# Optimization experiments

Measured on AMD Instinct MI355X. Metric: run time of the kernel, lower is better.

The kernel has to match this reference:

```python
import jax, jax.numpy as jnp
import numpy as np

T, B, E, H = 2048, 4, 1024, 16
HD = E // H
SCALE = HD ** -0.5


def setup_inputs() -> dict:
    key = jax.random.key(0)
    k1, k2, k3 = jax.random.split(key, 3)
    # xavier-ish scaling on weights for numerical sanity
    inputs = jax.random.normal(k1, (T, B, E), dtype=jnp.float32)
    in_proj_weight = jax.random.normal(k2, (3 * E, E), dtype=jnp.float32) * (2.0 / (4 * E)) ** 0.5
    out_proj_weight = jax.random.normal(k3, (E, E), dtype=jnp.float32) * (1.0 / E) ** 0.5
    return {"inputs": inputs, "in_proj_weight": in_proj_weight, "out_proj_weight": out_proj_weight}


def reference(inputs, in_proj_weight, out_proj_weight):
    t, b, e = inputs.shape
    # fused QKV projection: [T,B,E] @ [E,3E] -> [T, B*H, 3, HD]
    qkv = jnp.einsum('tbe,fe->tbf', inputs, in_proj_weight)
    qkv = qkv.reshape(t, b * H, 3, HD)
    q, k, v = qkv[:, :, 0, :], qkv[:, :, 1, :], qkv[:, :, 2, :]  # [T, B*H, HD]
    # scaled attention scores per (batch*head): [B*H, T, T]
    scores = SCALE * jnp.einsum('tnd,snd->nts', q, k)
    probs = jax.nn.softmax(scores, axis=-1)
    # dropout p=0.0 -> identity
    ctx = jnp.einsum('nts,snd->tnd', probs, v).reshape(t, b, e)
    # output projection (applied to attention context, matching intended math / backward)
    return jnp.einsum('tbe,oe->tbo', ctx, out_proj_weight)
```

## Files before the change

### kernel.cpp

```cpp
#include <hip/hip_runtime.h>
#include <stdint.h>
#include <stddef.h>


typedef __attribute__((ext_vector_type(8))) short bf16x8;
typedef __attribute__((ext_vector_type(4))) float f32x4;
typedef __attribute__((ext_vector_type(4))) unsigned int u32x4;

#define MFMA16(a, b, c) __builtin_amdgcn_mfma_f32_16x16x32_bf16((a), (b), (c), 0, 0, 0)

__device__ __forceinline__ unsigned short f2bf(float f) {
  unsigned u = __builtin_bit_cast(unsigned, f);
  u += 0x7fffu + ((u >> 16) & 1u);
  return (unsigned short)(u >> 16);
}

__device__ __forceinline__ float fast_exp2(float x) {
#if __has_builtin(__builtin_amdgcn_exp2f)
  return __builtin_amdgcn_exp2f(x);
#else
  return exp2f(x);
#endif
}

__device__ __forceinline__ unsigned cvtpk(float lo, float hi) {
  unsigned r;
  asm volatile("v_cvt_pk_bf16_f32 %0, %1, %2" : "=v"(r) : "v"(lo), "v"(hi));
  return r;
}

__device__ __forceinline__ void lane_swap32(unsigned &a, unsigned &b) {
#if __has_builtin(__builtin_amdgcn_permlane32_swap)
  auto r = __builtin_amdgcn_permlane32_swap(a, b, false, false);
  a = r[0]; b = r[1];
#else
  const bool hi = (threadIdx.x & 32) != 0;
  unsigned sa = (unsigned)__shfl_xor((int)a, 32, 64);
  unsigned sb = (unsigned)__shfl_xor((int)b, 32, 64);
  unsigned na = hi ? sb : a;
  unsigned nb = hi ? b : sa;
  a = na; b = nb;
#endif
}

__device__ __forceinline__ void lane_swap16(unsigned &a, unsigned &b) {
#if __has_builtin(__builtin_amdgcn_permlane16_swap)
  auto r = __builtin_amdgcn_permlane16_swap(a, b, false, false);
  a = r[0]; b = r[1];
#else
  const bool odd = (threadIdx.x & 16) != 0;
  unsigned sa = (unsigned)__shfl_xor((int)a, 16, 64);
  unsigned sb = (unsigned)__shfl_xor((int)b, 16, 64);
  unsigned na = odd ? sb : a;
  unsigned nb = odd ? b : sa;
  a = na; b = nb;
#endif
}

__device__ __forceinline__ void gload_lds16(const void* g, void* l) {
  __builtin_amdgcn_global_load_lds((const __attribute__((address_space(1))) void*)g,
                                   (__attribute__((address_space(3))) void*)l,
                                   16, 0, 0);
}

__global__ __launch_bounds__(256) void k_cvt(const float* __restrict__ src,
                                             unsigned short* __restrict__ dst, int n4) {
  int i = blockIdx.x * 256 + threadIdx.x;
  if (i >= n4) return;
  const float4 v = ((const float4*)src)[i];
  ushort4 o;
  o.x = f2bf(v.x); o.y = f2bf(v.y); o.z = f2bf(v.z); o.w = f2bf(v.w);
  ((ushort4*)dst)[i] = o;
}

__global__ __launch_bounds__(256, 2) void k_gemm_qkv(
    const unsigned short* __restrict__ A,
    const unsigned short* __restrict__ Bt,
    unsigned short* __restrict__ Qb,
    unsigned short* __restrict__ Kb,
    unsigned short* __restrict__ Vb) {
  constexpr int K = 1024;
  __shared__ __align__(16) unsigned short As[128 * 32];
  __shared__ __align__(16) unsigned short Bs[128 * 32];
  const int tid = threadIdx.x;
  const int l = tid & 63, w = tid >> 6;
  const int lr = l & 15, lg = l >> 4;
  const int bm = blockIdx.x, bn = blockIdx.y;
  const int wr = (w >> 1) * 64, wc = (w & 1) * 64;

  f32x4 acc[4][4] = {};

  const int o0 = tid * 16, o1 = tid * 16 + 4096;
  const int r0 = o0 >> 6, c0 = o0 & 63;
  const int r1 = o1 >> 6, c1 = o1 & 63;
  const char* gA0 = (const char*)A + (size_t)(bm * 128 + r0) * (K * 2) + c0;
  const char* gA1 = (const char*)A + (size_t)(bm * 128 + r1) * (K * 2) + c1;
  const char* gB0 = (const char*)Bt + (size_t)(bn * 128 + r0) * (K * 2) + c0;
  const char* gB1 = (const char*)Bt + (size_t)(bn * 128 + r1) * (K * 2) + c1;
  char* lA0 = (char*)As + o0;
  char* lA1 = (char*)As + o1;
  char* lB0 = (char*)Bs + o0;
  char* lB1 = (char*)Bs + o1;

  for (int kt = 0; kt < K / 32; ++kt) {
    const int kb = kt * 64;
    gload_lds16(gA0 + kb, lA0);
    gload_lds16(gA1 + kb, lA1);
    gload_lds16(gB0 + kb, lB0);
    gload_lds16(gB1 + kb, lB1);
    __syncthreads();
    bf16x8 af[4], bfr[4];
#pragma unroll
    for (int mf = 0; mf < 4; ++mf)
      af[mf] = *(const bf16x8*)&As[(wr + mf * 16 + lr) * 32 + lg * 8];
#pragma unroll
    for (int nf = 0; nf < 4; ++nf)
      bfr[nf] = *(const bf16x8*)&Bs[(wc + nf * 16 + lr) * 32 + lg * 8];
#pragma unroll
    for (int mf = 0; mf < 4; ++mf)
#pragma unroll
      for (int nf = 0; nf < 4; ++nf)
        acc[mf][nf] = MFMA16(af[mf], bfr[nf], acc[mf][nf]);
    __syncthreads();
  }

#pragma unroll
  for (int nf = 0; nf < 4; ++nf) {
    const int f = bn * 128 + wc + nf * 16 + lr;
    const int hq = f / 192;
    const int s3 = (f >> 6) % 3;
    const int d = f & 63;
    unsigned short* dst = (s3 == 0) ? Qb : (s3 == 1) ? Kb : Vb;
    const float qscale = (s3 == 0) ? 0.18033688011112042f : 1.0f;
#pragma unroll
    for (int mf = 0; mf < 4; ++mf) {
#pragma unroll
      for (int i = 0; i < 4; ++i) {
        const int r = bm * 128 + wr + mf * 16 + lg * 4 + i;
        const int t = r >> 2, bb2 = r & 3;
        const int nIdx = bb2 * 16 + hq;
        dst[((size_t)nIdx * 2048 + t) * 64 + d] = f2bf(acc[mf][nf][i] * qscale);
      }
    }
  }
}

__global__ __launch_bounds__(256) void k_vtrans(const unsigned short* __restrict__ V,
                                                unsigned short* __restrict__ VT) {
  __shared__ unsigned short tile[64][66];
  const int tid = threadIdx.x;
  const int n = blockIdx.y, t0 = blockIdx.x * 64;
  const int r = tid >> 2, c0 = (tid & 3) * 16;
  const unsigned short* src = V + ((size_t)(n * 2048 + t0 + r) * 64 + c0);
  bf16x8 a = *(const bf16x8*)src;
  bf16x8 b = *(const bf16x8*)(src + 8);
#pragma unroll
  for (int j = 0; j < 8; ++j) tile[r][c0 + j] = (unsigned short)a[j];
#pragma unroll
  for (int j = 0; j < 8; ++j) tile[r][c0 + 8 + j] = (unsigned short)b[j];
  __syncthreads();
  const int d = tid >> 2, u0 = (tid & 3) * 16;
  bf16x8 oA, oB;
#pragma unroll
  for (int j = 0; j < 8; ++j) oA[j] = (short)tile[u0 + j][d];
#pragma unroll
  for (int j = 0; j < 8; ++j) oB[j] = (short)tile[u0 + 8 + j][d];
  unsigned short* dst = VT + ((size_t)(n * 64 + d) * 2048 + t0 + u0);
  *(bf16x8*)dst = oA;
  *(bf16x8*)(dst + 8) = oB;
}

__global__ __launch_bounds__(256, 2) void k_attn(
    const unsigned short* __restrict__ Qb, const unsigned short* __restrict__ Kb,
    const unsigned short* __restrict__ VTb, unsigned short* __restrict__ Cx) {
  __shared__ __align__(16) unsigned short Ks[2][64 * 64];
  __shared__ __align__(16) unsigned short Vt[2][64 * 64];

  const int tid = threadIdx.x;
  const int l = tid & 63, w = tid >> 6;
  const int lq = l & 15, lg = l >> 4;
  const int n = blockIdx.x, qt = blockIdx.y;

  const unsigned short* Qh = Qb + (size_t)n * (2048 * 64);
  const unsigned short* Kh = Kb + (size_t)n * (2048 * 64);
  const unsigned short* Vh = VTb + (size_t)n * (64 * 2048);

  bf16x8 aq[4][2];
#pragma unroll
  for (int qf = 0; qf < 4; ++qf)
#pragma unroll
    for (int kd = 0; kd < 2; ++kd)
      aq[qf][kd] = *(const bf16x8*)&Qh[(size_t)(qt * 256 + w * 64 + qf * 16 + lq) * 64 +
                                       kd * 32 + lg * 8];

  f32x4 o[4][4] = {};
  float lsum[4] = {0.f, 0.f, 0.f, 0.f};

  char* Ksl = (char*)&Ks[0][0];
  char* Vtl = (char*)&Vt[0][0];

  auto STAGE = [&](int buf, int st) {
    const int s0 = st * 64;
#pragma unroll
    for (int it = 0; it < 2; ++it) {
      const int off = (it * 256 + tid) * 16;
      const int row = off >> 7;
      const int colb = (off & 127) ^ ((row & 7) << 4);
      gload_lds16((const char*)Kh + ((size_t)(s0 + row) << 7) + colb, Ksl + buf * 8192 + off);
      gload_lds16((const char*)Vh + ((size_t)row << 12) + (s0 << 1) + colb, Vtl + buf * 8192 + off);
    }
  };

  STAGE(0, 0);
  asm volatile("s_waitcnt vmcnt(0)" ::: "memory");
  __builtin_amdgcn_s_barrier();

#pragma unroll 2
  for (int st = 0; st < 32; ++st) {
    const int cur = st & 1;
    if (st + 1 < 32) STAGE(cur ^ 1, st + 1);

    const char* Kc = Ksl + cur * 8192;
    const char* Vc = Vtl + cur * 8192;

    __builtin_amdgcn_s_setprio(1);
#pragma unroll
    for (int kb = 0; kb < 2; ++kb) {
      bf16x8 kf[2][2];
#pragma unroll
      for (int sfl = 0; sfl < 2; ++sfl) {
        const int rowk = (2 * kb + sfl) * 16 + lq;
        const int sw = (rowk & 7) << 4;
        kf[sfl][0] = *(const bf16x8*)(Kc + ((rowk * 128 + lg * 16) ^ sw));
        kf[sfl][1] = *(const bf16x8*)(Kc + ((rowk * 128 + 64 + lg * 16) ^ sw));
      }

      bf16x8 pq[4];
#pragma unroll
      for (int qf = 0; qf < 4; ++qf) {
        f32x4 s0 = {0.f, 0.f, 0.f, 0.f};
        f32x4 s1 = {0.f, 0.f, 0.f, 0.f};
        s0 = MFMA16(kf[0][0], aq[qf][0], s0);
        s0 = MFMA16(kf[0][1], aq[qf][1], s0);
        s1 = MFMA16(kf[1][0], aq[qf][0], s1);
        s1 = MFMA16(kf[1][1], aq[qf][1], s1);
        float accs = 0.f;
#pragma unroll
        for (int i = 0; i < 4; ++i) {
          s0[i] = fast_exp2(s0[i]);
          s1[i] = fast_exp2(s1[i]);
          accs += s0[i] + s1[i];
        }
        lsum[qf] += accs;
        unsigned w0 = cvtpk(s0[0], s0[1]);
        unsigned w1 = cvtpk(s0[2], s0[3]);
        unsigned w2 = cvtpk(s1[0], s1[1]);
        unsigned w3 = cvtpk(s1[2], s1[3]);
        lane_swap32(w0, w2);
        lane_swap32(w1, w3);
        lane_swap16(w0, w2);
        lane_swap16(w1, w3);
        u32x4 t4 = {w0, w1, w2, w3};
        pq[qf] = __builtin_bit_cast(bf16x8, t4);
      }

#pragma unroll
      for (int df = 0; df < 4; ++df) {
        const int rowd = df * 16 + lq;
        const int sw = (rowd & 7) << 4;
        bf16x8 vf = *(const bf16x8*)(Vc + ((rowd * 128 + kb * 64 + lg * 16) ^ sw));
#pragma unroll
        for (int qf = 0; qf < 4; ++qf)
          o[df][qf] = MFMA16(vf, pq[qf], o[df][qf]);
      }
    }
    __builtin_amdgcn_s_setprio(0);

    asm volatile("s_waitcnt vmcnt(0)" ::: "memory");
    __builtin_amdgcn_s_barrier();
  }

  const int bb = n >> 4, h = n & 15;
#pragma unroll
  for (int qf = 0; qf < 4; ++qf) {
    float li = lsum[qf];
    li += __shfl_xor(li, 16, 64);
    li += __shfl_xor(li, 32, 64);
    const float inv = 1.0f / li;
    const int q = qt * 256 + w * 64 + qf * 16 + lq;
#pragma unroll
    for (int df = 0; df < 4; ++df) {
      ushort4 pk;
      pk.x = f2bf(o[df][qf][0] * inv);
      pk.y = f2bf(o[df][qf][1] * inv);
      pk.z = f2bf(o[df][qf][2] * inv);
      pk.w = f2bf(o[df][qf][3] * inv);
      *(ushort4*)&Cx[(size_t)(q * 4 + bb) * 1024 + h * 64 + df * 16 + lg * 4] = pk;
    }
  }
}

__global__ __launch_bounds__(256, 2) void k_gemm_out(
    const unsigned short* __restrict__ A,
    const unsigned short* __restrict__ Bt,
    float* __restrict__ C) {
  constexpr int K = 1024;
  __shared__ __align__(16) unsigned short As[128 * 32];
  __shared__ __align__(16) unsigned short Bs[128 * 32];
  const int tid = threadIdx.x;
  const int l = tid & 63, w = tid >> 6;
  const int lr = l & 15, lg = l >> 4;
  const int bm = blockIdx.x, bn = blockIdx.y;
  const int wr = (w >> 1) * 64, wc = (w & 1) * 64;

  f32x4 acc[4][4] = {};

  const int o0 = tid * 16, o1 = tid * 16 + 4096;
  const int r0 = o0 >> 6, c0 = o0 & 63;
  const int r1 = o1 >> 6, c1 = o1 & 63;
  const char* gA0 = (const char*)A + (size_t)(bm * 128 + r0) * (K * 2) + c0;
  const char* gA1 = (const char*)A + (size_t)(bm * 128 + r1) * (K * 2) + c1;
  const char* gB0 = (const char*)Bt + (size_t)(bn * 128 + r0) * (K * 2) + c0;
  const char* gB1 = (const char*)Bt + (size_t)(bn * 128 + r1) * (K * 2) + c1;
  char* lA0 = (char*)As + o0;
  char* lA1 = (char*)As + o1;
  char* lB0 = (char*)Bs + o0;
  char* lB1 = (char*)Bs + o1;

  for (int kt = 0; kt < K / 32; ++kt) {
    const int kb = kt * 64;
    gload_lds16(gA0 + kb, lA0);
    gload_lds16(gA1 + kb, lA1);
    gload_lds16(gB0 + kb, lB0);
    gload_lds16(gB1 + kb, lB1);
    __syncthreads();
    bf16x8 af[4], bfr[4];
#pragma unroll
    for (int mf = 0; mf < 4; ++mf)
      af[mf] = *(const bf16x8*)&As[(wr + mf * 16 + lr) * 32 + lg * 8];
#pragma unroll
    for (int nf = 0; nf < 4; ++nf)
      bfr[nf] = *(const bf16x8*)&Bs[(wc + nf * 16 + lr) * 32 + lg * 8];
#pragma unroll
    for (int mf = 0; mf < 4; ++mf)
#pragma unroll
      for (int nf = 0; nf < 4; ++nf)
        acc[mf][nf] = MFMA16(af[mf], bfr[nf], acc[mf][nf]);
    __syncthreads();
  }

#pragma unroll
  for (int mf = 0; mf < 4; ++mf)
#pragma unroll
    for (int i = 0; i < 4; ++i) {
      const int r = bm * 128 + wr + mf * 16 + lg * 4 + i;
#pragma unroll
      for (int nf = 0; nf < 4; ++nf)
        C[(size_t)r * 1024 + bn * 128 + wc + nf * 16 + lr] = acc[mf][nf][i];
    }
}

extern "C" void kernel_launch(void* const* d_in, const int* in_sizes, int n_in,
                              void* d_out, int out_size, void* d_ws, size_t ws_size,
                              hipStream_t stream) {
  const float* X = (const float*)d_in[0];
  const float* W1 = (const float*)d_in[1];
  const float* Wo = (const float*)d_in[2];
  float* out = (float*)d_out;

  char* ws = (char*)d_ws;
  unsigned short* Xb  = (unsigned short*)(ws);
  unsigned short* W1b = (unsigned short*)(ws + 16777216);
  unsigned short* Wob = (unsigned short*)(ws + 23068672);
  unsigned short* Qb  = (unsigned short*)(ws + 25165824);
  unsigned short* Kb  = (unsigned short*)(ws + 41943040);
  unsigned short* VTb = (unsigned short*)(ws + 58720256);
  unsigned short* Vb  = (unsigned short*)(ws + 75497472);
  unsigned short* Cx  = (unsigned short*)(ws + 75497472);

  k_cvt<<<8192, 256, 0, stream>>>(X, Xb, 2097152);
  k_cvt<<<3072, 256, 0, stream>>>(W1, W1b, 786432);
  k_cvt<<<1024, 256, 0, stream>>>(Wo, Wob, 262144);
  k_gemm_qkv<<<dim3(64, 24), 256, 0, stream>>>(Xb, W1b, Qb, Kb, Vb);
  k_vtrans<<<dim3(32, 64), 256, 0, stream>>>(Vb, VTb);
  k_attn<<<dim3(64, 8), 256, 0, stream>>>(Qb, Kb, VTb, Cx);
  k_gemm_out<<<dim3(64, 8), 256, 0, stream>>>(Cx, Wob, out);
}
```

Before: 197.9 us.

## Permute K row layout to drop lane swaps; stage 128-key tiles

Reorders which K rows each lane loads, using a new LDS swizzle, so the exp'd score fragments already sit in the lane layout the PV MFMA expects. This removes the permlane32/16 swap instructions from the inner loop. K/V staging tiles also double from 64 to 128 keys per stage, halving the number of barriers and loop iterations. LDS use doubles to 64KB per block, which may limit the two-blocks-per-CU occupancy target.

```diff
diff --git a/kernel.cpp b/kernel.cpp
--- a/kernel.cpp
+++ b/kernel.cpp
@@ -27,34 +27,6 @@
   unsigned r;
   asm volatile("v_cvt_pk_bf16_f32 %0, %1, %2" : "=v"(r) : "v"(lo), "v"(hi));
   return r;
-}
-
-__device__ __forceinline__ void lane_swap32(unsigned &a, unsigned &b) {
-#if __has_builtin(__builtin_amdgcn_permlane32_swap)
-  auto r = __builtin_amdgcn_permlane32_swap(a, b, false, false);
-  a = r[0]; b = r[1];
-#else
-  const bool hi = (threadIdx.x & 32) != 0;
-  unsigned sa = (unsigned)__shfl_xor((int)a, 32, 64);
-  unsigned sb = (unsigned)__shfl_xor((int)b, 32, 64);
-  unsigned na = hi ? sb : a;
-  unsigned nb = hi ? b : sa;
-  a = na; b = nb;
-#endif
-}
-
-__device__ __forceinline__ void lane_swap16(unsigned &a, unsigned &b) {
-#if __has_builtin(__builtin_amdgcn_permlane16_swap)
-  auto r = __builtin_amdgcn_permlane16_swap(a, b, false, false);
-  a = r[0]; b = r[1];
-#else
-  const bool odd = (threadIdx.x & 16) != 0;
-  unsigned sa = (unsigned)__shfl_xor((int)a, 16, 64);
-  unsigned sb = (unsigned)__shfl_xor((int)b, 16, 64);
-  unsigned na = odd ? sb : a;
-  unsigned nb = odd ? b : sa;
-  a = na; b = nb;
-#endif
 }
 
 __device__ __forceinline__ void gload_lds16(const void* g, void* l) {
@@ -173,8 +145,8 @@
 __global__ __launch_bounds__(256, 2) void k_attn(
     const unsigned short* __restrict__ Qb, const unsigned short* __restrict__ Kb,
     const unsigned short* __restrict__ VTb, unsigned short* __restrict__ Cx) {
-  __shared__ __align__(16) unsigned short Ks[2][64 * 64];
-  __shared__ __align__(16) unsigned short Vt[2][64 * 64];
+  __shared__ __align__(16) unsigned short Ks[2][128 * 64];
+  __shared__ __align__(16) unsigned short Vt[2][64 * 128];
 
   const int tid = threadIdx.x;
   const int l = tid & 63, w = tid >> 6;
@@ -199,15 +171,30 @@
   char* Ksl = (char*)&Ks[0][0];
   char* Vtl = (char*)&Vt[0][0];
 
+  const int swzK = (((lq & 3) | (((lq >> 2) & 1) << 2)) << 4);
+  const int colK0 = (lg * 16) ^ swzK;
+  const int colK1 = (64 + lg * 16) ^ swzK;
+  const int rowbase = (lq >> 2) * 8 + (lq & 3);
+  const int swzV = (lq & 7) << 4;
+
   auto STAGE = [&](int buf, int st) {
-    const int s0 = st * 64;
-#pragma unroll
-    for (int it = 0; it < 2; ++it) {
+    const int s0 = st * 128;
+#pragma unroll
+    for (int it = 0; it < 4; ++it) {
       const int off = (it * 256 + tid) * 16;
       const int row = off >> 7;
-      const int colb = (off & 127) ^ ((row & 7) << 4);
-      gload_lds16((const char*)Kh + ((size_t)(s0 + row) << 7) + colb, Ksl + buf * 8192 + off);
-      gload_lds16((const char*)Vh + ((size_t)row << 12) + (s0 << 1) + colb, Vtl + buf * 8192 + off);
+      const int col = off & 127;
+      const int g = (row & 3) | (((row >> 3) & 1) << 2);
+      gload_lds16((const char*)Kh + ((size_t)(s0 + row) << 7) + (col ^ (g << 4)),
+                  Ksl + buf * 16384 + off);
+    }
+#pragma unroll
+    for (int it = 0; it < 4; ++it) {
+      const int off = (it * 256 + tid) * 16;
+      const int row = off >> 8;
+      const int col = off & 255;
+      gload_lds16((const char*)Vh + ((size_t)row << 12) + (s0 << 1) + (col ^ ((row & 7) << 4)),
+                  Vtl + buf * 16384 + off);
     }
   };
 
@@ -216,59 +203,49 @@
   __builtin_amdgcn_s_barrier();
 
 #pragma unroll 2
-  for (int st = 0; st < 32; ++st) {
-    const int cur = st & 1;
-    if (st + 1 < 32) STAGE(cur ^ 1, st + 1);
-
-    const char* Kc = Ksl + cur * 8192;
-    const char* Vc = Vtl + cur * 8192;
+  for (int st = 0; st < 16; ++st) {
+    if (st + 1 < 16) STAGE((st + 1) & 1, st + 1);
+
+    const char* Kc = Ksl + (st & 1) * 16384;
+    const char* Vc = Vtl + (st & 1) * 16384;
 
     __builtin_amdgcn_s_setprio(1);
 #pragma unroll
-    for (int kb = 0; kb < 2; ++kb) {
+    for (int kb = 0; kb < 4; ++kb) {
       bf16x8 kf[2][2];
 #pragma unroll
-      for (int sfl = 0; sfl < 2; ++sfl) {
-        const int rowk = (2 * kb + sfl) * 16 + lq;
-        const int sw = (rowk & 7) << 4;
-        kf[sfl][0] = *(const bf16x8*)(Kc + ((rowk * 128 + lg * 16) ^ sw));
-        kf[sfl][1] = *(const bf16x8*)(Kc + ((rowk * 128 + 64 + lg * 16) ^ sw));
+      for (int f = 0; f < 2; ++f) {
+        const int row = kb * 32 + rowbase + f * 4;
+        kf[f][0] = *(const bf16x8*)(Kc + row * 128 + colK0);
+        kf[f][1] = *(const bf16x8*)(Kc + row * 128 + colK1);
       }
 
       bf16x8 pq[4];
 #pragma unroll
       for (int qf = 0; qf < 4; ++qf) {
-        f32x4 s0 = {0.f, 0.f, 0.f, 0.f};
         f32x4 s1 = {0.f, 0.f, 0.f, 0.f};
-        s0 = MFMA16(kf[0][0], aq[qf][0], s0);
-        s0 = MFMA16(kf[0][1], aq[qf][1], s0);
-        s1 = MFMA16(kf[1][0], aq[qf][0], s1);
-        s1 = MFMA16(kf[1][1], aq[qf][1], s1);
+        f32x4 s2 = {0.f, 0.f, 0.f, 0.f};
+        s1 = MFMA16(kf[0][0], aq[qf][0], s1);
+        s1 = MFMA16(kf[0][1], aq[qf][1], s1);
+        s2 = MFMA16(kf[1][0], aq[qf][0], s2);
+        s2 = MFMA16(kf[1][1], aq[qf][1], s2);
         float accs = 0.f;
 #pragma unroll
         for (int i = 0; i < 4; ++i) {
-          s0[i] = fast_exp2(s0[i]);
           s1[i] = fast_exp2(s1[i]);
-          accs += s0[i] + s1[i];
+          s2[i] = fast_exp2(s2[i]);
+          accs += s1[i] + s2[i];
         }
         lsum[qf] += accs;
-        unsigned w0 = cvtpk(s0[0], s0[1]);
-        unsigned w1 = cvtpk(s0[2], s0[3]);
-        unsigned w2 = cvtpk(s1[0], s1[1]);
-        unsigned w3 = cvtpk(s1[2], s1[3]);
-        lane_swap32(w0, w2);
-        lane_swap32(w1, w3);
-        lane_swap16(w0, w2);
-        lane_swap16(w1, w3);
-        u32x4 t4 = {w0, w1, w2, w3};
+        u32x4 t4 = {cvtpk(s1[0], s1[1]), cvtpk(s1[2], s1[3]),
+                    cvtpk(s2[0], s2[1]), cvtpk(s2[2], s2[3])};
         pq[qf] = __builtin_bit_cast(bf16x8, t4);
       }
 
 #pragma unroll
       for (int df = 0; df < 4; ++df) {
         const int rowd = df * 16 + lq;
-        const int sw = (rowd & 7) << 4;
-        bf16x8 vf = *(const bf16x8*)(Vc + ((rowd * 128 + kb * 64 + lg * 16) ^ sw));
+        bf16x8 vf = *(const bf16x8*)(Vc + rowd * 256 + ((kb * 64 + lg * 16) ^ swzV));
 #pragma unroll
         for (int qf = 0; qf < 4; ++qf)
           o[df][qf] = MFMA16(vf, pq[qf], o[df][qf]);
```

After: 222.0 us. +12.2%, slower.

## Rewrite QKV GEMM with 256x256 tiles, double-buffered swizzled LDS and interleaved staging

Applied to the files above, without the earlier changes.

The QKV projection GEMM moves from 128x128 tiles with 4 waves and single-buffered LDS to 256x256 tiles with 8 waves. LDS buffers are double-buffered and XOR-swizzled, and the next K-tile's global-to-LDS loads are interleaved with the MFMA phases under s_setprio. The goal is to raise data reuse per tile, hide global load latency, and avoid LDS bank conflicts. The cost is much larger LDS use, which limits occupancy, and a 384-block grid that fills the CUs unevenly.

```diff
diff --git a/kernel.cpp b/kernel.cpp
--- a/kernel.cpp
+++ b/kernel.cpp
@@ -63,6 +63,8 @@
                                    16, 0, 0);
 }
 
+__device__ __forceinline__ void cfence() { asm volatile("" ::: "memory"); }
+
 __global__ __launch_bounds__(256) void k_cvt(const float* __restrict__ src,
                                              unsigned short* __restrict__ dst, int n4) {
   int i = blockIdx.x * 256 + threadIdx.x;
@@ -73,73 +75,143 @@
   ((ushort4*)dst)[i] = o;
 }
 
-__global__ __launch_bounds__(256, 2) void k_gemm_qkv(
+__global__ __launch_bounds__(512, 2) void k_gemm_qkv(
     const unsigned short* __restrict__ A,
     const unsigned short* __restrict__ Bt,
     unsigned short* __restrict__ Qb,
     unsigned short* __restrict__ Kb,
     unsigned short* __restrict__ Vb) {
-  constexpr int K = 1024;
-  __shared__ __align__(16) unsigned short As[128 * 32];
-  __shared__ __align__(16) unsigned short Bs[128 * 32];
+  __shared__ __align__(16) unsigned short As[2][2][256 * 32];
+  __shared__ __align__(16) unsigned short Bs[2][2][256 * 32];
+
   const int tid = threadIdx.x;
-  const int l = tid & 63, w = tid >> 6;
+  const int l = tid & 63;
+  const int wid = tid >> 6;
   const int lr = l & 15, lg = l >> 4;
+  const int wr = wid >> 2, wc = wid & 3;
   const int bm = blockIdx.x, bn = blockIdx.y;
-  const int wr = (w >> 1) * 64, wc = (w & 1) * 64;
-
-  f32x4 acc[4][4] = {};
-
-  const int o0 = tid * 16, o1 = tid * 16 + 4096;
-  const int r0 = o0 >> 6, c0 = o0 & 63;
-  const int r1 = o1 >> 6, c1 = o1 & 63;
-  const char* gA0 = (const char*)A + (size_t)(bm * 128 + r0) * (K * 2) + c0;
-  const char* gA1 = (const char*)A + (size_t)(bm * 128 + r1) * (K * 2) + c1;
-  const char* gB0 = (const char*)Bt + (size_t)(bn * 128 + r0) * (K * 2) + c0;
-  const char* gB1 = (const char*)Bt + (size_t)(bn * 128 + r1) * (K * 2) + c1;
-  char* lA0 = (char*)As + o0;
-  char* lA1 = (char*)As + o1;
-  char* lB0 = (char*)Bs + o0;
-  char* lB1 = (char*)Bs + o1;
-
-  for (int kt = 0; kt < K / 32; ++kt) {
-    const int kb = kt * 64;
-    gload_lds16(gA0 + kb, lA0);
-    gload_lds16(gA1 + kb, lA1);
-    gload_lds16(gB0 + kb, lB0);
-    gload_lds16(gB1 + kb, lB1);
-    __syncthreads();
-    bf16x8 af[4], bfr[4];
-#pragma unroll
-    for (int mf = 0; mf < 4; ++mf)
-      af[mf] = *(const bf16x8*)&As[(wr + mf * 16 + lr) * 32 + lg * 8];
-#pragma unroll
-    for (int nf = 0; nf < 4; ++nf)
-      bfr[nf] = *(const bf16x8*)&Bs[(wc + nf * 16 + lr) * 32 + lg * 8];
-#pragma unroll
-    for (int mf = 0; mf < 4; ++mf)
-#pragma unroll
-      for (int nf = 0; nf < 4; ++nf)
-        acc[mf][nf] = MFMA16(af[mf], bfr[nf], acc[mf][nf]);
-    __syncthreads();
+
+  f32x4 acc[8][4] = {};
+
+  const int colF = (lg * 16) ^ (((lr >> 1) & 3) << 4);
+
+  auto STAGE = [&](unsigned short* lds_unit, const unsigned short* gbase, int grow0,
+                   int kt2, int uk) {
+#pragma unroll
+    for (int i = 0; i < 2; ++i) {
+      const int idx = i * 512 + tid;
+      const int row = idx >> 2;
+      const int colb = (idx & 3) * 16;
+      const int sw = ((row >> 1) & 3) << 4;
+      gload_lds16((const char*)gbase + (size_t)(grow0 + row) * 2048 + kt2 * 128 +
+                      uk * 64 + (colb ^ sw),
+                  (char*)lds_unit + idx * 16);
+    }
+  };
+
+  auto LDA4 = [&](int buf, int uk, int mhalf, bf16x8* d) {
+#pragma unroll
+    for (int mf = 0; mf < 4; ++mf) {
+      const int row = wr * 128 + (mhalf * 4 + mf) * 16 + lr;
+      d[mf] = *(const bf16x8*)((const char*)&As[buf][uk][0] + row * 64 + colF);
+    }
+  };
+  auto LDB4 = [&](int buf, int uk, bf16x8* d) {
+#pragma unroll
+    for (int nf = 0; nf < 4; ++nf) {
+      const int row = wc * 64 + nf * 16 + lr;
+      d[nf] = *(const bf16x8*)((const char*)&Bs[buf][uk][0] + row * 64 + colF);
+    }
+  };
+
+  STAGE(&As[0][0][0], A, bm * 256, 0, 0);
+  STAGE(&Bs[0][0][0], Bt, bn * 256, 0, 0);
+  STAGE(&As[0][1][0], A, bm * 256, 0, 1);
+  STAGE(&Bs[0][1][0], Bt, bn * 256, 0, 1);
+  asm volatile("s_waitcnt vmcnt(4)" ::: "memory");
+  __builtin_amdgcn_s_barrier();
+  cfence();
+
+#pragma unroll 2
+  for (int kt = 0; kt < 16; ++kt) {
+    const int buf = kt & 1, nbuf = buf ^ 1;
+    const int ktn = (kt + 1 < 16) ? kt + 1 : 15;
+
+    bf16x8 a0[4], b0[4];
+    LDA4(buf, 0, 0, a0);
+    LDB4(buf, 0, b0);
+    STAGE(&As[nbuf][0][0], A, bm * 256, ktn, 0);
+    __builtin_amdgcn_s_setprio(1);
+#pragma unroll
+    for (int mf = 0; mf < 4; ++mf)
+#pragma unroll
+      for (int nf = 0; nf < 4; ++nf)
+        acc[mf][nf] = MFMA16(a0[mf], b0[nf], acc[mf][nf]);
+    __builtin_amdgcn_s_setprio(0);
+    cfence();
+    __builtin_amdgcn_s_barrier();
+    cfence();
+
+    bf16x8 a1[4];
+    LDA4(buf, 0, 1, a1);
+    STAGE(&Bs[nbuf][0][0], Bt, bn * 256, ktn, 0);
+    __builtin_amdgcn_s_setprio(1);
+#pragma unroll
+    for (int mf = 0; mf < 4; ++mf)
+#pragma unroll
+      for (int nf = 0; nf < 4; ++nf)
+        acc[4 + mf][nf] = MFMA16(a1[mf], b0[nf], acc[4 + mf][nf]);
+    __builtin_amdgcn_s_setprio(0);
+    asm volatile("s_waitcnt vmcnt(4)" ::: "memory");
+    __builtin_amdgcn_s_barrier();
+    cfence();
+
+    bf16x8 a2[4], b1[4];
+    LDA4(buf, 1, 0, a2);
+    LDB4(buf, 1, b1);
+    STAGE(&As[nbuf][1][0], A, bm * 256, ktn, 1);
+    __builtin_amdgcn_s_setprio(1);
+#pragma unroll
+    for (int mf = 0; mf < 4; ++mf)
+#pragma unroll
+      for (int nf = 0; nf < 4; ++nf)
+        acc[mf][nf] = MFMA16(a2[mf], b1[nf], acc[mf][nf]);
+    __builtin_amdgcn_s_setprio(0);
+    cfence();
+    __builtin_amdgcn_s_barrier();
+    cfence();
+
+    bf16x8 a3[4];
+    LDA4(buf, 1, 1, a3);
+    STAGE(&Bs[nbuf][1][0], Bt, bn * 256, ktn, 1);
+    __builtin_amdgcn_s_setprio(1);
+#pragma unroll
+    for (int mf = 0; mf < 4; ++mf)
+#pragma unroll
+      for (int nf = 0; nf < 4; ++nf)
+        acc[4 + mf][nf] = MFMA16(a3[mf], b1[nf], acc[4 + mf][nf]);
+    __builtin_amdgcn_s_setprio(0);
+    asm volatile("s_waitcnt vmcnt(4)" ::: "memory");
+    __builtin_amdgcn_s_barrier();
+    cfence();
   }
 
 #pragma unroll
   for (int nf = 0; nf < 4; ++nf) {
-    const int f = bn * 128 + wc + nf * 16 + lr;
+    const int f = bn * 256 + wc * 64 + nf * 16 + lr;
     const int hq = f / 192;
     const int s3 = (f >> 6) % 3;
     const int d = f & 63;
     unsigned short* dst = (s3 == 0) ? Qb : (s3 == 1) ? Kb : Vb;
     const float qscale = (s3 == 0) ? 0.18033688011112042f : 1.0f;
 #pragma unroll
-    for (int mf = 0; mf < 4; ++mf) {
+    for (int mq = 0; mq < 8; ++mq) {
 #pragma unroll
       for (int i = 0; i < 4; ++i) {
-        const int r = bm * 128 + wr + mf * 16 + lg * 4 + i;
+        const int r = bm * 256 + wr * 128 + mq * 16 + lg * 4 + i;
         const int t = r >> 2, bb2 = r & 3;
         const int nIdx = bb2 * 16 + hq;
-        dst[((size_t)nIdx * 2048 + t) * 64 + d] = f2bf(acc[mf][nf][i] * qscale);
+        dst[((size_t)nIdx * 2048 + t) * 64 + d] = f2bf(acc[mq][nf][i] * qscale);
       }
     }
   }
@@ -381,7 +453,7 @@
   k_cvt<<<8192, 256, 0, stream>>>(X, Xb, 2097152);
   k_cvt<<<3072, 256, 0, stream>>>(W1, W1b, 786432);
   k_cvt<<<1024, 256, 0, stream>>>(Wo, Wob, 262144);
-  k_gemm_qkv<<<dim3(64, 24), 256, 0, stream>>>(Xb, W1b, Qb, Kb, Vb);
+  k_gemm_qkv<<<dim3(32, 12), 512, 0, stream>>>(Xb, W1b, Qb, Kb, Vb);
   k_vtrans<<<dim3(32, 64), 256, 0, stream>>>(Vb, VTb);
   k_attn<<<dim3(64, 8), 256, 0, stream>>>(Qb, Kb, VTb, Cx);
   k_gemm_out<<<dim3(64, 8), 256, 0, stream>>>(Cx, Wob, out);
```

New measurement: 199.9 us. No clear change (+1.0%).

## Use single-wave attention blocks without barriers and merge conversion kernels

Applied to the files above, without the earlier changes.

The attention kernel moves from 4-wave blocks that share K/V tiles to 1-wave blocks, each handling 64 queries, with a 32-key stage depth and a new V swizzle. This removes the workgroup barriers, and the grid grows from 512 to 2048 blocks to give more scheduling freedom. In exchange each wave loads its own K/V, so global/L2 traffic for K and V rises fourfold. The three fp32-to-bf16 conversion launches are also merged into one kernel to cut launch overhead.

```diff
diff --git a/kernel.cpp b/kernel.cpp
--- a/kernel.cpp
+++ b/kernel.cpp
@@ -63,14 +63,23 @@
                                    16, 0, 0);
 }
 
-__global__ __launch_bounds__(256) void k_cvt(const float* __restrict__ src,
-                                             unsigned short* __restrict__ dst, int n4) {
+__global__ __launch_bounds__(256) void k_cvt3(const float* __restrict__ X,
+                                              const float* __restrict__ W1,
+                                              const float* __restrict__ Wo,
+                                              unsigned short* __restrict__ Xb,
+                                              unsigned short* __restrict__ W1b,
+                                              unsigned short* __restrict__ Wob) {
   int i = blockIdx.x * 256 + threadIdx.x;
-  if (i >= n4) return;
-  const float4 v = ((const float4*)src)[i];
+  const float* src;
+  unsigned short* dst;
+  int j;
+  if (i < 2097152) { src = X; dst = Xb; j = i; }
+  else if (i < 2097152 + 786432) { src = W1; dst = W1b; j = i - 2097152; }
+  else { src = Wo; dst = Wob; j = i - (2097152 + 786432); }
+  const float4 v = ((const float4*)src)[j];
   ushort4 o;
   o.x = f2bf(v.x); o.y = f2bf(v.y); o.z = f2bf(v.z); o.w = f2bf(v.w);
-  ((ushort4*)dst)[i] = o;
+  ((ushort4*)dst)[j] = o;
 }
 
 __global__ __launch_bounds__(256, 2) void k_gemm_qkv(
@@ -170,14 +179,13 @@
   *(bf16x8*)(dst + 8) = oB;
 }
 
-__global__ __launch_bounds__(256, 2) void k_attn(
+__global__ __launch_bounds__(64, 2) void k_attn(
     const unsigned short* __restrict__ Qb, const unsigned short* __restrict__ Kb,
     const unsigned short* __restrict__ VTb, unsigned short* __restrict__ Cx) {
-  __shared__ __align__(16) unsigned short Ks[2][64 * 64];
-  __shared__ __align__(16) unsigned short Vt[2][64 * 64];
-
-  const int tid = threadIdx.x;
-  const int l = tid & 63, w = tid >> 6;
+  __shared__ __align__(16) unsigned short Ks[2][32 * 64];
+  __shared__ __align__(16) unsigned short Vt[2][64 * 32];
+
+  const int l = threadIdx.x;
   const int lq = l & 15, lg = l >> 4;
   const int n = blockIdx.x, qt = blockIdx.y;
 
@@ -190,94 +198,94 @@
   for (int qf = 0; qf < 4; ++qf)
 #pragma unroll
     for (int kd = 0; kd < 2; ++kd)
-      aq[qf][kd] = *(const bf16x8*)&Qh[(size_t)(qt * 256 + w * 64 + qf * 16 + lq) * 64 +
+      aq[qf][kd] = *(const bf16x8*)&Qh[(size_t)(qt * 64 + qf * 16 + lq) * 64 +
                                        kd * 32 + lg * 8];
 
   f32x4 o[4][4] = {};
   float lsum[4] = {0.f, 0.f, 0.f, 0.f};
 
-  char* Ksl = (char*)&Ks[0][0];
-  char* Vtl = (char*)&Vt[0][0];
+  char* KsB = (char*)&Ks[0][0];
+  char* VtB = (char*)&Vt[0][0];
 
   auto STAGE = [&](int buf, int st) {
-    const int s0 = st * 64;
-#pragma unroll
-    for (int it = 0; it < 2; ++it) {
-      const int off = (it * 256 + tid) * 16;
-      const int row = off >> 7;
-      const int colb = (off & 127) ^ ((row & 7) << 4);
-      gload_lds16((const char*)Kh + ((size_t)(s0 + row) << 7) + colb, Ksl + buf * 8192 + off);
-      gload_lds16((const char*)Vh + ((size_t)row << 12) + (s0 << 1) + colb, Vtl + buf * 8192 + off);
+    const int s0 = st * 32;
+#pragma unroll
+    for (int it = 0; it < 4; ++it) {
+      const int idx = it * 64 + l;
+      const int krow = idx >> 3;
+      const int kcol = (idx & 7) * 16;
+      gload_lds16((const char*)Kh + ((size_t)(s0 + krow) << 7) + (kcol ^ ((krow & 7) << 4)),
+                  KsB + buf * 4096 + idx * 16);
+      const int vrow = idx >> 2;
+      const int vcol = (idx & 3) * 16;
+      gload_lds16((const char*)Vh + ((size_t)vrow << 12) + (s0 << 1) +
+                      (vcol ^ (((vrow >> 1) & 3) << 4)),
+                  VtB + buf * 4096 + idx * 16);
     }
   };
 
   STAGE(0, 0);
   asm volatile("s_waitcnt vmcnt(0)" ::: "memory");
-  __builtin_amdgcn_s_barrier();
 
 #pragma unroll 2
-  for (int st = 0; st < 32; ++st) {
+  for (int st = 0; st < 64; ++st) {
     const int cur = st & 1;
-    if (st + 1 < 32) STAGE(cur ^ 1, st + 1);
-
-    const char* Kc = Ksl + cur * 8192;
-    const char* Vc = Vtl + cur * 8192;
+    if (st + 1 < 64) STAGE(cur ^ 1, st + 1);
+
+    const char* Kc = KsB + cur * 4096;
+    const char* Vc = VtB + cur * 4096;
 
     __builtin_amdgcn_s_setprio(1);
-#pragma unroll
-    for (int kb = 0; kb < 2; ++kb) {
-      bf16x8 kf[2][2];
-#pragma unroll
-      for (int sfl = 0; sfl < 2; ++sfl) {
-        const int rowk = (2 * kb + sfl) * 16 + lq;
-        const int sw = (rowk & 7) << 4;
-        kf[sfl][0] = *(const bf16x8*)(Kc + ((rowk * 128 + lg * 16) ^ sw));
-        kf[sfl][1] = *(const bf16x8*)(Kc + ((rowk * 128 + 64 + lg * 16) ^ sw));
+    bf16x8 kf[2][2];
+#pragma unroll
+    for (int sfl = 0; sfl < 2; ++sfl) {
+      const int rowk = sfl * 16 + lq;
+      const int sw = (rowk & 7) << 4;
+      kf[sfl][0] = *(const bf16x8*)(Kc + ((rowk * 128 + lg * 16) ^ sw));
+      kf[sfl][1] = *(const bf16x8*)(Kc + ((rowk * 128 + 64 + lg * 16) ^ sw));
+    }
+
+    bf16x8 pq[4];
+#pragma unroll
+    for (int qf = 0; qf < 4; ++qf) {
+      f32x4 s0 = {0.f, 0.f, 0.f, 0.f};
+      f32x4 s1 = {0.f, 0.f, 0.f, 0.f};
+      s0 = MFMA16(kf[0][0], aq[qf][0], s0);
+      s0 = MFMA16(kf[0][1], aq[qf][1], s0);
+      s1 = MFMA16(kf[1][0], aq[qf][0], s1);
+      s1 = MFMA16(kf[1][1], aq[qf][1], s1);
+      float accs = 0.f;
+#pragma unroll
+      for (int i = 0; i < 4; ++i) {
+        s0[i] = fast_exp2(s0[i]);
+        s1[i] = fast_exp2(s1[i]);
+        accs += s0[i] + s1[i];
       }
-
-      bf16x8 pq[4];
-#pragma unroll
-      for (int qf = 0; qf < 4; ++qf) {
-        f32x4 s0 = {0.f, 0.f, 0.f, 0.f};
-        f32x4 s1 = {0.f, 0.f, 0.f, 0.f};
-        s0 = MFMA16(kf[0][0], aq[qf][0], s0);
-        s0 = MFMA16(kf[0][1], aq[qf][1], s0);
-        s1 = MFMA16(kf[1][0], aq[qf][0], s1);
-        s1 = MFMA16(kf[1][1], aq[qf][1], s1);
-        float accs = 0.f;
-#pragma unroll
-        for (int i = 0; i < 4; ++i) {
-          s0[i] = fast_exp2(s0[i]);
-          s1[i] = fast_exp2(s1[i]);
-          accs += s0[i] + s1[i];
-        }
-        lsum[qf] += accs;
-        unsigned w0 = cvtpk(s0[0], s0[1]);
-        unsigned w1 = cvtpk(s0[2], s0[3]);
-        unsigned w2 = cvtpk(s1[0], s1[1]);
-        unsigned w3 = cvtpk(s1[2], s1[3]);
-        lane_swap32(w0, w2);
-        lane_swap32(w1, w3);
-        lane_swap16(w0, w2);
-        lane_swap16(w1, w3);
-        u32x4 t4 = {w0, w1, w2, w3};
-        pq[qf] = __builtin_bit_cast(bf16x8, t4);
-      }
-
-#pragma unroll
-      for (int df = 0; df < 4; ++df) {
-        const int rowd = df * 16 + lq;
-        const int sw = (rowd & 7) << 4;
-        bf16x8 vf = *(const bf16x8*)(Vc + ((rowd * 128 + kb * 64 + lg * 16) ^ sw));
-#pragma unroll
-        for (int qf = 0; qf < 4; ++qf)
-          o[df][qf] = MFMA16(vf, pq[qf], o[df][qf]);
-      }
+      lsum[qf] += accs;
+      unsigned w0 = cvtpk(s0[0], s0[1]);
+      unsigned w1 = cvtpk(s0[2], s0[3]);
+      unsigned w2 = cvtpk(s1[0], s1[1]);
+      unsigned w3 = cvtpk(s1[2], s1[3]);
+      lane_swap32(w0, w2);
+      lane_swap32(w1, w3);
+      lane_swap16(w0, w2);
+      lane_swap16(w1, w3);
+      u32x4 t4 = {w0, w1, w2, w3};
+      pq[qf] = __builtin_bit_cast(bf16x8, t4);
+    }
+
+#pragma unroll
+    for (int df = 0; df < 4; ++df) {
+      const int rowd = df * 16 + lq;
+      const int sw = ((rowd >> 1) & 3) << 4;
+      bf16x8 vf = *(const bf16x8*)(Vc + ((rowd * 64 + lg * 16) ^ sw));
+#pragma unroll
+      for (int qf = 0; qf < 4; ++qf)
+        o[df][qf] = MFMA16(vf, pq[qf], o[df][qf]);
     }
     __builtin_amdgcn_s_setprio(0);
 
     asm volatile("s_waitcnt vmcnt(0)" ::: "memory");
-    __builtin_amdgcn_s_barrier();
   }
 
   const int bb = n >> 4, h = n & 15;
@@ -287,7 +295,7 @@
     li += __shfl_xor(li, 16, 64);
     li += __shfl_xor(li, 32, 64);
     const float inv = 1.0f / li;
-    const int q = qt * 256 + w * 64 + qf * 16 + lq;
+    const int q = qt * 64 + qf * 16 + lq;
 #pragma unroll
     for (int df = 0; df < 4; ++df) {
       ushort4 pk;
@@ -378,11 +386,9 @@
   unsigned short* Vb  = (unsigned short*)(ws + 75497472);
   unsigned short* Cx  = (unsigned short*)(ws + 75497472);
 
-  k_cvt<<<8192, 256, 0, stream>>>(X, Xb, 2097152);
-  k_cvt<<<3072, 256, 0, stream>>>(W1, W1b, 786432);
-  k_cvt<<<1024, 256, 0, stream>>>(Wo, Wob, 262144);
+  k_cvt3<<<12288, 256, 0, stream>>>(X, W1, Wo, Xb, W1b, Wob);
   k_gemm_qkv<<<dim3(64, 24), 256, 0, stream>>>(Xb, W1b, Qb, Kb, Vb);
   k_vtrans<<<dim3(32, 64), 256, 0, stream>>>(Vb, VTb);
-  k_attn<<<dim3(64, 8), 256, 0, stream>>>(Qb, Kb, VTb, Cx);
+  k_attn<<<dim3(64, 32), 64, 0, stream>>>(Qb, Kb, VTb, Cx);
   k_gemm_out<<<dim3(64, 8), 256, 0, stream>>>(Cx, Wob, out);
 }
```

After: 202.6 us. 2.4% more time.
